# Kernel tuning notes

Hardware: AMD Instinct MI355X
Metric: run time of the kernel (lower is better)

The kernel has to match this reference:

```python
import jax, jax.numpy as jnp
import numpy as np

D = 256
B, N1, N2 = 4, 512, 512


def setup_inputs() -> dict:
    key = jax.random.key(0)
    k = jax.random.split(key, 6)
    s1 = 1.0 / np.sqrt(2 * D)  # torch Linear init bound ~ U(-1/sqrt(fan_in), ...)
    s2 = 1.0 / np.sqrt(D)
    return {
        "x": jax.random.normal(k[0], (B, N1, D), jnp.float32),
        "y": jax.random.normal(k[1], (B, N2, D), jnp.float32),
        "W1": jax.random.uniform(k[2], (2 * D, D), jnp.float32, -s1, s1),  # linear1.weight.T
        "b1": jax.random.uniform(k[3], (D,), jnp.float32, -s1, s1),
        "W2": jax.random.uniform(k[4], (D, 1), jnp.float32, -s2, s2),  # out.weight.T
        "b2": jax.random.uniform(k[5], (1,), jnp.float32, -s2, s2),
    }


def reference(x, y, W1, b1, W2, b2):
    # linear1 over concat([x,y]) is separable: split W1 into x-part and y-part,
    # project each sequence once, then broadcast-sum over the (n1, n2) grid.
    Wx, Wy = W1[:D], W1[D:]                     # [d, d] each
    xp = jnp.einsum('bnd,de->bne', x, Wx)       # [b, n1, d]
    yp = jnp.einsum('bmd,de->bme', y, Wy)       # [b, n2, d]
    h = xp[:, :, None, :] + yp[:, None, :, :] + b1  # [b, n1, n2, d]
    h = jax.nn.gelu(h, approximate=False)       # torch nn.GELU() is exact erf
    o = jnp.einsum('bnmd,de->bnme', h, W2) + b2  # [b, n1, n2, 1]
    return o[..., 0]                             # [b, n1, n2]
```

## Files before the change

### kernel.cpp

```cpp
#include <hip/hip_runtime.h>

#define DD 256
#define N1 512
#define N2 512
#define BB 4

typedef float f2 __attribute__((ext_vector_type(2)));

__global__ __launch_bounds__(256) void proj_kernel(
    const float* __restrict__ x, const float* __restrict__ y,
    const float* __restrict__ W1, const float* __restrict__ b1,
    float* __restrict__ xp, float* __restrict__ yp)
{
    const int which = blockIdx.z;
    const float* __restrict__ A  = which ? y : x;
    const float* __restrict__ Bw = W1 + which * DD * DD;
    float* __restrict__ outp = which ? yp : xp;

    __shared__ float As[32 * 36];
    __shared__ float Bs[32 * 68];

    const int tid = threadIdx.x;
    const int tx = tid & 15, ty = tid >> 4;
    const int mBase = blockIdx.x * 32;
    const int nBase = blockIdx.y * 64;

    const float4* A4 = (const float4*)A;
    const float4* B4 = (const float4*)Bw;

    const int ar = tid >> 3;
    const int ac = tid & 7;
    const int br = tid >> 4;
    const int bc = tid & 15;

    float4 pa, pb0, pb1;
    pa  = A4[(mBase + ar) * 64 + 0 * 8 + ac];
    pb0 = B4[(0 * 32 + br) * 64 + (nBase >> 2) + bc];
    pb1 = B4[(0 * 32 + br + 16) * 64 + (nBase >> 2) + bc];

    float acc[2][4] = {};

    for (int kc = 0; kc < 8; ++kc) {
        __syncthreads();
        {
            float av[4] = {pa.x, pa.y, pa.z, pa.w};
            #pragma unroll
            for (int q = 0; q < 4; ++q) As[(ac * 4 + q) * 36 + ar] = av[q];
            *(float4*)&Bs[br * 68 + bc * 4] = pb0;
            *(float4*)&Bs[(br + 16) * 68 + bc * 4] = pb1;
        }
        __syncthreads();
        if (kc < 7) {
            pa  = A4[(mBase + ar) * 64 + (kc + 1) * 8 + ac];
            pb0 = B4[((kc + 1) * 32 + br) * 64 + (nBase >> 2) + bc];
            pb1 = B4[((kc + 1) * 32 + br + 16) * 64 + (nBase >> 2) + bc];
        }
        #pragma unroll
        for (int k = 0; k < 32; ++k) {
            float2 a = *(const float2*)&As[k * 36 + ty * 2];
            float4 b = *(const float4*)&Bs[k * 68 + tx * 4];
            float av[2] = {a.x, a.y};
            float bv[4] = {b.x, b.y, b.z, b.w};
            #pragma unroll
            for (int i = 0; i < 2; ++i)
                #pragma unroll
                for (int j = 0; j < 4; ++j)
                    acc[i][j] = fmaf(av[i], bv[j], acc[i][j]);
        }
    }

    float4 bias = make_float4(0.f, 0.f, 0.f, 0.f);
    if (which == 0) bias = *((const float4*)b1 + (nBase >> 2) + tx);
    #pragma unroll
    for (int i = 0; i < 2; ++i) {
        float4 o;
        o.x = acc[i][0] + bias.x;
        o.y = acc[i][1] + bias.y;
        o.z = acc[i][2] + bias.z;
        o.w = acc[i][3] + bias.w;
        ((float4*)outp)[(mBase + ty * 2 + i) * (DD / 4) + (nBase >> 2) + tx] = o;
    }
}

__device__ __forceinline__ f2 gelu2(f2 h)
{
    f2 h2 = h * h;
    f2 t  = __builtin_elementwise_fma(h2, (f2)0.1029432f, (f2)2.3022083f);
    f2 z  = h * t;
    f2 e;
    e.x = __builtin_amdgcn_exp2f(z.x);
    e.y = __builtin_amdgcn_exp2f(z.y);
    f2 a = e + 1.0f;
    f2 r;
    r.x = __builtin_amdgcn_rcpf(a.x);
    r.y = __builtin_amdgcn_rcpf(a.y);
    return __builtin_elementwise_fma(-h, r, h);
}

__global__ __launch_bounds__(256, 4) void cross_kernel(
    const float* __restrict__ xp, const float* __restrict__ yp,
    const float* __restrict__ W2, const float* __restrict__ b2,
    float* __restrict__ o)
{
    __shared__ float xs[32 * 68];
    __shared__ float ys[32 * 68];

    const int tid   = threadIdx.x;
    const int b     = blockIdx.z;
    const int mBase = blockIdx.x * 32;
    const int nBase = blockIdx.y * 32;
    const int tx = tid & 15;
    const int ty = tid >> 4;

    const float4* xp4 = (const float4*)xp + (b * N1 + nBase) * (DD / 4);
    const float4* yp4 = (const float4*)yp + (b * N2 + mBase) * (DD / 4);
    const float4* __restrict__ W2v = (const float4*)W2;

    const int srow = tid >> 4;
    const int sc4  = tid & 15;

    float4 px[2], py[2];
    px[0] = xp4[srow * 64 + 0 * 16 + sc4];
    px[1] = xp4[(srow + 16) * 64 + 0 * 16 + sc4];
    py[0] = yp4[srow * 64 + 0 * 16 + sc4];
    py[1] = yp4[(srow + 16) * 64 + 0 * 16 + sc4];

    f2 acc[2][2] = {};

    for (int kc = 0; kc < 4; ++kc) {
        __syncthreads();
        *(float4*)&xs[srow * 68 + sc4 * 4]        = px[0];
        *(float4*)&xs[(srow + 16) * 68 + sc4 * 4] = px[1];
        *(float4*)&ys[srow * 68 + sc4 * 4]        = py[0];
        *(float4*)&ys[(srow + 16) * 68 + sc4 * 4] = py[1];
        __syncthreads();
        if (kc < 3) {
            px[0] = xp4[srow * 64 + (kc + 1) * 16 + sc4];
            px[1] = xp4[(srow + 16) * 64 + (kc + 1) * 16 + sc4];
            py[0] = yp4[srow * 64 + (kc + 1) * 16 + sc4];
            py[1] = yp4[(srow + 16) * 64 + (kc + 1) * 16 + sc4];
        }

        #pragma unroll
        for (int c4 = 0; c4 < 16; ++c4) {
            float4 wv = W2v[kc * 16 + c4];
            f2 wlo = {wv.x, wv.y};
            f2 whi = {wv.z, wv.w};
            float4 xr[2], yr[2];
            #pragma unroll
            for (int i = 0; i < 2; ++i)
                xr[i] = *(const float4*)&xs[(ty + 16 * i) * 68 + c4 * 4];
            #pragma unroll
            for (int j = 0; j < 2; ++j)
                yr[j] = *(const float4*)&ys[(tx + 16 * j) * 68 + c4 * 4];
            #pragma unroll
            for (int i = 0; i < 2; ++i) {
                f2 xlo = {xr[i].x, xr[i].y};
                f2 xhi = {xr[i].z, xr[i].w};
                #pragma unroll
                for (int j = 0; j < 2; ++j) {
                    f2 ylo = {yr[j].x, yr[j].y};
                    f2 yhi = {yr[j].z, yr[j].w};
                    f2 glo = gelu2(xlo + ylo);
                    acc[i][j] = __builtin_elementwise_fma(glo, wlo, acc[i][j]);
                    f2 ghi = gelu2(xhi + yhi);
                    acc[i][j] = __builtin_elementwise_fma(ghi, whi, acc[i][j]);
                }
            }
        }
    }

    const float bias2 = b2[0];
    const size_t base = ((size_t)(b * N1 + nBase)) * N2 + mBase;
    #pragma unroll
    for (int i = 0; i < 2; ++i) {
        #pragma unroll
        for (int j = 0; j < 2; ++j) {
            o[base + (size_t)(ty + 16 * i) * N2 + (tx + 16 * j)] =
                acc[i][j].x + acc[i][j].y + bias2;
        }
    }
}

extern "C" void kernel_launch(void* const* d_in, const int* in_sizes, int n_in,
                              void* d_out, int out_size, void* d_ws, size_t ws_size,
                              hipStream_t stream)
{
    const float* x  = (const float*)d_in[0];
    const float* y  = (const float*)d_in[1];
    const float* W1 = (const float*)d_in[2];
    const float* b1 = (const float*)d_in[3];
    const float* W2 = (const float*)d_in[4];
    const float* b2 = (const float*)d_in[5];
    float* o  = (float*)d_out;
    float* xp = (float*)d_ws;
    float* yp = xp + (BB * N1) * DD;

    dim3 g1(64, 4, 2);
    proj_kernel<<<g1, 256, 0, stream>>>(x, y, W1, b1, xp, yp);

    dim3 g2(N2 / 32, N1 / 32, BB);
    cross_kernel<<<g2, 256, 0, stream>>>(xp, yp, W2, b2, o);
}
```

Baseline: 142.0 us.

## Restructure cross kernel: transposed y tile in LDS, x rows read directly from global

```diff
diff --git a/kernel.cpp b/kernel.cpp
--- a/kernel.cpp
+++ b/kernel.cpp
@@ -34,9 +34,9 @@
     const int bc = tid & 15;
 
     float4 pa, pb0, pb1;
-    pa  = A4[(mBase + ar) * 64 + 0 * 8 + ac];
-    pb0 = B4[(0 * 32 + br) * 64 + (nBase >> 2) + bc];
-    pb1 = B4[(0 * 32 + br + 16) * 64 + (nBase >> 2) + bc];
+    pa  = A4[(mBase + ar) * 64 + ac];
+    pb0 = B4[br * 64 + (nBase >> 2) + bc];
+    pb1 = B4[(br + 16) * 64 + (nBase >> 2) + bc];
 
     float acc[2][4] = {};
 
@@ -102,83 +102,94 @@
     const float* __restrict__ W2, const float* __restrict__ b2,
     float* __restrict__ o)
 {
-    __shared__ float xs[32 * 68];
-    __shared__ float ys[32 * 68];
+    __shared__ float yt[256 * 32];
 
     const int tid   = threadIdx.x;
     const int b     = blockIdx.z;
     const int mBase = blockIdx.x * 32;
     const int nBase = blockIdx.y * 32;
-    const int tx = tid & 15;
-    const int ty = tid >> 4;
-
-    const float4* xp4 = (const float4*)xp + (b * N1 + nBase) * (DD / 4);
-    const float4* yp4 = (const float4*)yp + (b * N2 + mBase) * (DD / 4);
+
+    {
+        const int m    = tid & 31;
+        const int dblk = tid >> 5;
+        const float4* src = (const float4*)yp
+                          + ((size_t)(b * N2 + mBase + m)) * 64 + dblk * 8;
+        #pragma unroll
+        for (int k = 0; k < 8; ++k) {
+            float4 v = src[k];
+            int d0 = dblk * 32 + k * 4;
+            yt[(d0 + 0) * 32 + m] = v.x;
+            yt[(d0 + 1) * 32 + m] = v.y;
+            yt[(d0 + 2) * 32 + m] = v.z;
+            yt[(d0 + 3) * 32 + m] = v.w;
+        }
+    }
+    __syncthreads();
+
+    const int wave = tid >> 6;
+    const int lane = tid & 63;
+    const int m    = lane & 31;
+    const int half = lane >> 5;
+    const int n0   = nBase + wave * 8 + half * 4;
+
+    const float4* x4 = (const float4*)(xp + ((size_t)(b * N1 + n0)) * DD);
     const float4* __restrict__ W2v = (const float4*)W2;
 
-    const int srow = tid >> 4;
-    const int sc4  = tid & 15;
-
-    float4 px[2], py[2];
-    px[0] = xp4[srow * 64 + 0 * 16 + sc4];
-    px[1] = xp4[(srow + 16) * 64 + 0 * 16 + sc4];
-    py[0] = yp4[srow * 64 + 0 * 16 + sc4];
-    py[1] = yp4[(srow + 16) * 64 + 0 * 16 + sc4];
-
-    f2 acc[2][2] = {};
-
-    for (int kc = 0; kc < 4; ++kc) {
-        __syncthreads();
-        *(float4*)&xs[srow * 68 + sc4 * 4]        = px[0];
-        *(float4*)&xs[(srow + 16) * 68 + sc4 * 4] = px[1];
-        *(float4*)&ys[srow * 68 + sc4 * 4]        = py[0];
-        *(float4*)&ys[(srow + 16) * 68 + sc4 * 4] = py[1];
-        __syncthreads();
-        if (kc < 3) {
-            px[0] = xp4[srow * 64 + (kc + 1) * 16 + sc4];
-            px[1] = xp4[(srow + 16) * 64 + (kc + 1) * 16 + sc4];
-            py[0] = yp4[srow * 64 + (kc + 1) * 16 + sc4];
-            py[1] = yp4[(srow + 16) * 64 + (kc + 1) * 16 + sc4];
-        }
-
+    f2 acc[4] = {};
+    float4 xa[4], xb[4];
+    #pragma unroll
+    for (int j = 0; j < 4; ++j) xa[j] = x4[j * 64 + 0];
+    float4 wcur = W2v[0];
+
+    for (int g = 0; g < 64; g += 2) {
         #pragma unroll
-        for (int c4 = 0; c4 < 16; ++c4) {
-            float4 wv = W2v[kc * 16 + c4];
-            f2 wlo = {wv.x, wv.y};
-            f2 whi = {wv.z, wv.w};
-            float4 xr[2], yr[2];
-            #pragma unroll
-            for (int i = 0; i < 2; ++i)
-                xr[i] = *(const float4*)&xs[(ty + 16 * i) * 68 + c4 * 4];
-            #pragma unroll
-            for (int j = 0; j < 2; ++j)
-                yr[j] = *(const float4*)&ys[(tx + 16 * j) * 68 + c4 * 4];
-            #pragma unroll
-            for (int i = 0; i < 2; ++i) {
-                f2 xlo = {xr[i].x, xr[i].y};
-                f2 xhi = {xr[i].z, xr[i].w};
-                #pragma unroll
-                for (int j = 0; j < 2; ++j) {
-                    f2 ylo = {yr[j].x, yr[j].y};
-                    f2 yhi = {yr[j].z, yr[j].w};
-                    f2 glo = gelu2(xlo + ylo);
-                    acc[i][j] = __builtin_elementwise_fma(glo, wlo, acc[i][j]);
-                    f2 ghi = gelu2(xhi + yhi);
-                    acc[i][j] = __builtin_elementwise_fma(ghi, whi, acc[i][j]);
-                }
+        for (int j = 0; j < 4; ++j) xb[j] = x4[j * 64 + g + 1];
+        float4 wnxt = W2v[g + 1];
+        {
+            const int d0 = g * 4;
+            f2 y01 = { yt[(d0 + 0) * 32 + m], yt[(d0 + 1) * 32 + m] };
+            f2 y23 = { yt[(d0 + 2) * 32 + m], yt[(d0 + 3) * 32 + m] };
+            f2 wlo = {wcur.x, wcur.y};
+            f2 whi = {wcur.z, wcur.w};
+            #pragma unroll
+            for (int j = 0; j < 4; ++j) {
+                f2 xlo = {xa[j].x, xa[j].y};
+                f2 xhi = {xa[j].z, xa[j].w};
+                f2 glo = gelu2(xlo + y01);
+                acc[j] = __builtin_elementwise_fma(glo, wlo, acc[j]);
+                f2 ghi = gelu2(xhi + y23);
+                acc[j] = __builtin_elementwise_fma(ghi, whi, acc[j]);
             }
         }
+        if (g < 62) {
+            #pragma unroll
+            for (int j = 0; j < 4; ++j) xa[j] = x4[j * 64 + g + 2];
+        }
+        float4 wnn = (g < 62) ? W2v[g + 2] : wnxt;
+        {
+            const int d0 = (g + 1) * 4;
+            f2 y01 = { yt[(d0 + 0) * 32 + m], yt[(d0 + 1) * 32 + m] };
+            f2 y23 = { yt[(d0 + 2) * 32 + m], yt[(d0 + 3) * 32 + m] };
+            f2 wlo = {wnxt.x, wnxt.y};
+            f2 whi = {wnxt.z, wnxt.w};
+            #pragma unroll
+            for (int j = 0; j < 4; ++j) {
+                f2 xlo = {xb[j].x, xb[j].y};
+                f2 xhi = {xb[j].z, xb[j].w};
+                f2 glo = gelu2(xlo + y01);
+                acc[j] = __builtin_elementwise_fma(glo, wlo, acc[j]);
+                f2 ghi = gelu2(xhi + y23);
+                acc[j] = __builtin_elementwise_fma(ghi, whi, acc[j]);
+            }
+        }
+        wcur = wnn;
     }
 
     const float bias2 = b2[0];
-    const size_t base = ((size_t)(b * N1 + nBase)) * N2 + mBase;
+    float* ob = o + (size_t)b * N1 * N2;
     #pragma unroll
-    for (int i = 0; i < 2; ++i) {
-        #pragma unroll
-        for (int j = 0; j < 2; ++j) {
-            o[base + (size_t)(ty + 16 * i) * N2 + (tx + 16 * j)] =
-                acc[i][j].x + acc[i][j].y + bias2;
-        }
+    for (int j = 0; j < 4; ++j) {
+        ob[(size_t)(n0 + j) * N2 + mBase + m] = acc[j].x + acc[j].y + bias2;
     }
 }
 
```

Result: slower. 154.0 us (+8.5%).
